# Optimization experiments

Hardware: AMD Instinct MI355X
Metric: run time of the kernel (lower is better)

## Reference

```python
import jax, jax.numpy as jnp
import numpy as np

INPUT_DIM = 1024
OUTPUT_DIM = 1024
DEGREE = 8


def setup_inputs() -> dict:
    key = jax.random.key(0)
    k1, k2 = jax.random.split(key)
    x = jax.random.normal(k1, (8192, INPUT_DIM), dtype=jnp.float32)
    std = 1.0 / (INPUT_DIM * (DEGREE + 1))
    cheby_coeffs = std * jax.random.normal(k2, (INPUT_DIM, OUTPUT_DIM, DEGREE + 1), dtype=jnp.float32)
    return {"x": x, "cheby_coeffs": cheby_coeffs}


def reference(x, cheby_coeffs):
    # x: (B, I); cheby_coeffs: (I, O, D+1)
    degree = cheby_coeffs.shape[-1] - 1
    xt = jnp.tanh(x.reshape(-1, cheby_coeffs.shape[0]))
    # Chebyshev recurrence T_0=1, T_1=x, T_k = 2*x*T_{k-1} - T_{k-2}
    polys = [jnp.ones_like(xt)]
    if degree > 0:
        polys.append(xt)
    for _ in range(2, degree + 1):
        polys.append(2.0 * xt * polys[-1] - polys[-2])
    cheby = jnp.stack(polys, axis=-1)  # (B, I, D+1)
    y = jnp.einsum('bid,iod->bo', cheby, cheby_coeffs)
    return y
```

## Files before the change

kernel.cpp:

```cpp
#include <hip/hip_runtime.h>
#include <hip/hip_bf16.h>

#define AS1 __attribute__((address_space(1)))
#define AS3 __attribute__((address_space(3)))

typedef __attribute__((ext_vector_type(8))) short bf16x8;
typedef __attribute__((ext_vector_type(4))) float f32x4;

#define CSTRIDE 9216
#define KT2 8192
#define NOUT 1024

__device__ __forceinline__ void gll16(const void* g, void* l) {
    __builtin_amdgcn_global_load_lds((const AS1 void*)g, (AS3 void*)l, 16, 0, 0);
}
static __device__ __forceinline__ unsigned short f2bf(float f) {
    union { __hip_bfloat16 h; unsigned short u; } cv;
    cv.h = __float2bfloat16(f);
    return cv.u;
}
static __device__ __forceinline__ float bf2f(unsigned short u) {
    union { float f; unsigned v; } c; c.v = (unsigned)u << 16; return c.f;
}
static __device__ __forceinline__ float fast_tanhf(float v) {
    float e = __expf(2.0f * v);
    return 1.0f - 2.0f / (e + 1.0f);
}

__global__ void __launch_bounds__(256) prep_kernel(const float* __restrict__ cc,
                                                   unsigned short* __restrict__ Wt,
                                                   float* __restrict__ bias) {
    __shared__ unsigned short T[288 * 68];
    const int t  = threadIdx.x;
    const int n0 = (blockIdx.x & 31) * 32;
    const int i0 = (blockIdx.x >> 5) * 64;

    for (int il = 0; il < 64; ++il) {
        const float* src = cc + (size_t)(i0 + il) * CSTRIDE + (size_t)n0 * 9;
        for (int f = t; f < 288; f += 256)
            T[f * 68 + il] = f2bf(src[f]);
    }
    __syncthreads();

#pragma unroll
    for (int it = 0; it < 16; ++it) {
        const int chunk = it * 16 + (t >> 4);
        const int nl = chunk >> 3;
        const int dd = chunk & 7;
        const int n  = n0 + nl;
        const int e0 = (t & 15) * 4;
        const int isrc = e0 ^ ((n & 7) << 3);
        ushort4 v = *(const ushort4*)&T[(nl * 9 + dd + 1) * 68 + isrc];
        *(ushort4*)(Wt + (size_t)n * KT2 + dd * 1024 + i0 + e0) = v;
    }

    if (t < 32) {
        float s = 0.f;
#pragma unroll 8
        for (int il = 0; il < 64; ++il) s += bf2f(T[(t * 9) * 68 + il]);
        atomicAdd(&bias[n0 + t], s);
    }
}

__global__ void __launch_bounds__(256, 2)
cheby_gemm(const float* __restrict__ x, const unsigned short* __restrict__ Wt,
           const float* __restrict__ bias, float* __restrict__ out) {
    __shared__ unsigned short Asub[128 * 64];
    __shared__ unsigned short Bsub[2][128 * 64];

    const int id   = blockIdx.x;
    const int bcol = (id & 7) * 128;
    const int brow = (id >> 3) * 128;
    const int t    = threadIdx.x;
    const int lane = t & 63;
    const int w    = t >> 6;
    const int wr   = (w >> 1) * 64;
    const int wc   = (w & 1) * 64;
    const int l15  = lane & 15;
    const int lhi  = lane >> 4;

    const int gi0 = (t & 15) * 4;
    const int gr  = t >> 4;
    const int bn_loc = t >> 3;
    const int bpos   = (t & 7) * 8;

    unsigned awoff[8];
#pragma unroll
    for (int p = 0; p < 8; ++p) {
        const int r = gr + 16 * p;
        awoff[p] = r * 128 + ((gi0 * 2) ^ ((r & 7) << 4));
    }

    f32x4 acc[4][4] = {};
    float x2[8][4], Tp[8][4], Tpp[8][4];
    float4 xt[8];

#pragma unroll
    for (int p = 0; p < 8; ++p)
        xt[p] = *(const float4*)(x + (size_t)(brow + gr + 16 * p) * 1024 + gi0);
#pragma unroll
    for (int c = 0; c < 4; ++c)
        gll16(Wt + (size_t)(bcol + c * 32 + bn_loc) * KT2 + bpos,
              (char*)Bsub[0] + c * 4096 + w * 1024);

#pragma unroll 1
    for (int ic = 0; ic < 16; ++ic) {
#pragma unroll
        for (int dd = 0; dd < 8; ++dd) {
            const int cur = dd & 1;
            const int nxt = cur ^ 1;
            const int ddn = (dd + 1) & 7;
            const int icn = (dd == 7) ? ((ic + 1) & 15) : ic;
            const int kbn = ddn * 1024 + icn * 64;

            __builtin_amdgcn_s_barrier();

            const bool xpre = (dd == 7) && (ic != 15);
            if (xpre) {
#pragma unroll
                for (int p = 0; p < 8; ++p)
                    xt[p] = *(const float4*)(x + (size_t)(brow + gr + 16 * p) * 1024
                                             + icn * 64 + gi0);
            }

#pragma unroll
            for (int c = 0; c < 4; ++c)
                gll16(Wt + (size_t)(bcol + c * 32 + bn_loc) * KT2 + kbn + bpos,
                      (char*)Bsub[nxt] + c * 4096 + w * 1024);

            if (dd == 0) {
#pragma unroll
                for (int p = 0; p < 8; ++p) {
                    ushort4 pk; unsigned short* pks = (unsigned short*)&pk;
#pragma unroll
                    for (int j = 0; j < 4; ++j) {
                        x2[p][j] = 2.0f * fast_tanhf((&xt[p].x)[j]);
                        const float c = 0.5f * x2[p][j];
                        Tp[p][j] = c; Tpp[p][j] = 1.0f;
                        pks[j] = f2bf(c);
                    }
                    *(ushort4*)((char*)Asub + awoff[p]) = pk;
                }
            } else {
#pragma unroll
                for (int p = 0; p < 8; ++p) {
                    ushort4 pk; unsigned short* pks = (unsigned short*)&pk;
#pragma unroll
                    for (int j = 0; j < 4; ++j) {
                        const float c = __builtin_fmaf(x2[p][j], Tp[p][j], -Tpp[p][j]);
                        Tpp[p][j] = Tp[p][j]; Tp[p][j] = c;
                        pks[j] = f2bf(c);
                    }
                    *(ushort4*)((char*)Asub + awoff[p]) = pk;
                }
            }

            if (xpre) {
                asm volatile("s_waitcnt vmcnt(12) lgkmcnt(0)" ::: "memory");
            } else {
                asm volatile("s_waitcnt vmcnt(4) lgkmcnt(0)" ::: "memory");
            }
            __builtin_amdgcn_s_barrier();

#pragma unroll
            for (int ks = 0; ks < 2; ++ks) {
                bf16x8 af[4], bfr[4];
#pragma unroll
                for (int mf = 0; mf < 4; ++mf) {
                    const int row = wr + mf * 16 + l15;
                    af[mf] = *(const bf16x8*)((const char*)Asub + row * 128 +
                              ((ks * 64 + lhi * 16) ^ ((row & 7) << 4)));
                }
#pragma unroll
                for (int nf = 0; nf < 4; ++nf) {
                    const int n = wc + nf * 16 + l15;
                    bfr[nf] = *(const bf16x8*)((const char*)Bsub[cur] + n * 128 +
                              ((ks * 64 + lhi * 16) ^ ((n & 7) << 4)));
                }
#pragma unroll
                for (int mf = 0; mf < 4; ++mf)
#pragma unroll
                    for (int nf = 0; nf < 4; ++nf)
                        acc[mf][nf] = __builtin_amdgcn_mfma_f32_16x16x32_bf16(
                            af[mf], bfr[nf], acc[mf][nf], 0, 0, 0);
            }
        }
    }

    float bv[4];
#pragma unroll
    for (int nf = 0; nf < 4; ++nf) bv[nf] = bias[bcol + wc + nf * 16 + l15];
#pragma unroll
    for (int mf = 0; mf < 4; ++mf)
#pragma unroll
        for (int nf = 0; nf < 4; ++nf)
#pragma unroll
            for (int ri = 0; ri < 4; ++ri) {
                const int orow = brow + wr + mf * 16 + lhi * 4 + ri;
                const int ocol = bcol + wc + nf * 16 + l15;
                out[(size_t)orow * NOUT + ocol] = acc[mf][nf][ri] + bv[nf];
            }
}

__global__ void __launch_bounds__(256) naive_kernel(const float* __restrict__ x,
                                                    const float* __restrict__ cc,
                                                    float* __restrict__ out) {
    __shared__ float xs[1024];
    const int b = blockIdx.x;
    const int t = threadIdx.x;
#pragma unroll
    for (int j = 0; j < 4; ++j)
        xs[t * 4 + j] = fast_tanhf(x[(size_t)b * 1024 + t * 4 + j]);
    __syncthreads();

    const int o = t * 4;
    float a0 = 0.f, a1 = 0.f, a2 = 0.f, a3 = 0.f;
    for (int i = 0; i < 1024; ++i) {
        const float* cp = cc + (size_t)i * CSTRIDE + (size_t)o * 9;
        const float xv = xs[i];
        float tpp = 1.0f, tp = xv;
        a0 += cp[0];  a1 += cp[9];  a2 += cp[18];  a3 += cp[27];
        a0 += xv * cp[1]; a1 += xv * cp[10]; a2 += xv * cp[19]; a3 += xv * cp[28];
#pragma unroll
        for (int d = 2; d <= 8; ++d) {
            const float cur = 2.0f * xv * tp - tpp;
            tpp = tp; tp = cur;
            a0 += cur * cp[d];      a1 += cur * cp[9 + d];
            a2 += cur * cp[18 + d]; a3 += cur * cp[27 + d];
        }
    }
    float* op = out + (size_t)b * NOUT + o;
    op[0] = a0; op[1] = a1; op[2] = a2; op[3] = a3;
}

extern "C" void kernel_launch(void* const* d_in, const int* in_sizes, int n_in,
                              void* d_out, int out_size, void* d_ws, size_t ws_size,
                              hipStream_t stream) {
    const float* x  = (const float*)d_in[0];
    const float* cc = (const float*)d_in[1];
    float* out = (float*)d_out;

    const size_t wt_bytes = (size_t)KT2 * 1024 * sizeof(unsigned short);
    const size_t need = wt_bytes + 1024 * sizeof(float);
    if (ws_size >= need) {
        unsigned short* Wt = (unsigned short*)d_ws;
        float* bias = (float*)((char*)d_ws + wt_bytes);
        hipMemsetAsync(bias, 0, 1024 * sizeof(float), stream);
        prep_kernel<<<512, 256, 0, stream>>>(cc, Wt, bias);
        cheby_gemm<<<512, 256, 0, stream>>>(x, Wt, bias, out);
    } else {
        naive_kernel<<<8192, 256, 0, stream>>>(x, cc, out);
    }
}
```

Baseline: 274.3 us.

## Shrink GEMM M-tile to 64 and drop B double buffering for occupancy

Halves the row tile of the Chebyshev GEMM to 64, removes the double-buffered B tile and the cross-iteration x prefetch, and launches twice as many blocks with launch bounds raised to 4 waves per SIMD. The aim is to raise occupancy by cutting LDS and register use so that more resident blocks hide latency. In exchange, loads are no longer overlapped within a block, each W tile is fetched twice as often, and every step waits on a full synchronization.

```diff
diff --git a/kernel.cpp b/kernel.cpp
--- a/kernel.cpp
+++ b/kernel.cpp
@@ -62,19 +62,19 @@
     }
 }
 
-__global__ void __launch_bounds__(256, 2)
+__global__ void __launch_bounds__(256, 4)
 cheby_gemm(const float* __restrict__ x, const unsigned short* __restrict__ Wt,
            const float* __restrict__ bias, float* __restrict__ out) {
-    __shared__ unsigned short Asub[128 * 64];
-    __shared__ unsigned short Bsub[2][128 * 64];
+    __shared__ unsigned short Asub[64 * 64];
+    __shared__ unsigned short Bsub[128 * 64];
 
     const int id   = blockIdx.x;
     const int bcol = (id & 7) * 128;
-    const int brow = (id >> 3) * 128;
+    const int brow = (id >> 3) * 64;
     const int t    = threadIdx.x;
     const int lane = t & 63;
     const int w    = t >> 6;
-    const int wr   = (w >> 1) * 64;
+    const int wr   = (w >> 1) * 32;
     const int wc   = (w & 1) * 64;
     const int l15  = lane & 15;
     const int lhi  = lane >> 4;
@@ -84,53 +84,37 @@
     const int bn_loc = t >> 3;
     const int bpos   = (t & 7) * 8;
 
-    unsigned awoff[8];
-#pragma unroll
-    for (int p = 0; p < 8; ++p) {
+    unsigned awoff[4];
+#pragma unroll
+    for (int p = 0; p < 4; ++p) {
         const int r = gr + 16 * p;
         awoff[p] = r * 128 + ((gi0 * 2) ^ ((r & 7) << 4));
     }
 
-    f32x4 acc[4][4] = {};
-    float x2[8][4], Tp[8][4], Tpp[8][4];
-    float4 xt[8];
-
-#pragma unroll
-    for (int p = 0; p < 8; ++p)
-        xt[p] = *(const float4*)(x + (size_t)(brow + gr + 16 * p) * 1024 + gi0);
-#pragma unroll
-    for (int c = 0; c < 4; ++c)
-        gll16(Wt + (size_t)(bcol + c * 32 + bn_loc) * KT2 + bpos,
-              (char*)Bsub[0] + c * 4096 + w * 1024);
+    f32x4 acc[2][4] = {};
+    float x2[4][4], Tp[4][4], Tpp[4][4];
 
 #pragma unroll 1
     for (int ic = 0; ic < 16; ++ic) {
+        float4 xt[4];
+#pragma unroll
+        for (int p = 0; p < 4; ++p)
+            xt[p] = *(const float4*)(x + (size_t)(brow + gr + 16 * p) * 1024
+                                     + ic * 64 + gi0);
+
 #pragma unroll
         for (int dd = 0; dd < 8; ++dd) {
-            const int cur = dd & 1;
-            const int nxt = cur ^ 1;
-            const int ddn = (dd + 1) & 7;
-            const int icn = (dd == 7) ? ((ic + 1) & 15) : ic;
-            const int kbn = ddn * 1024 + icn * 64;
-
-            __builtin_amdgcn_s_barrier();
-
-            const bool xpre = (dd == 7) && (ic != 15);
-            if (xpre) {
-#pragma unroll
-                for (int p = 0; p < 8; ++p)
-                    xt[p] = *(const float4*)(x + (size_t)(brow + gr + 16 * p) * 1024
-                                             + icn * 64 + gi0);
-            }
-
+            __syncthreads();
+
+            const int kb = dd * 1024 + ic * 64;
 #pragma unroll
             for (int c = 0; c < 4; ++c)
-                gll16(Wt + (size_t)(bcol + c * 32 + bn_loc) * KT2 + kbn + bpos,
-                      (char*)Bsub[nxt] + c * 4096 + w * 1024);
+                gll16(Wt + (size_t)(bcol + c * 32 + bn_loc) * KT2 + kb + bpos,
+                      (char*)Bsub + c * 4096 + w * 1024);
 
             if (dd == 0) {
 #pragma unroll
-                for (int p = 0; p < 8; ++p) {
+                for (int p = 0; p < 4; ++p) {
                     ushort4 pk; unsigned short* pks = (unsigned short*)&pk;
 #pragma unroll
                     for (int j = 0; j < 4; ++j) {
@@ -143,7 +127,7 @@
                 }
             } else {
 #pragma unroll
-                for (int p = 0; p < 8; ++p) {
+                for (int p = 0; p < 4; ++p) {
                     ushort4 pk; unsigned short* pks = (unsigned short*)&pk;
 #pragma unroll
                     for (int j = 0; j < 4; ++j) {
@@ -155,18 +139,13 @@
                 }
             }
 
-            if (xpre) {
-                asm volatile("s_waitcnt vmcnt(12) lgkmcnt(0)" ::: "memory");
-            } else {
-                asm volatile("s_waitcnt vmcnt(4) lgkmcnt(0)" ::: "memory");
-            }
-            __builtin_amdgcn_s_barrier();
+            __syncthreads();
 
 #pragma unroll
             for (int ks = 0; ks < 2; ++ks) {
-                bf16x8 af[4], bfr[4];
-#pragma unroll
-                for (int mf = 0; mf < 4; ++mf) {
+                bf16x8 af[2], bfr[4];
+#pragma unroll
+                for (int mf = 0; mf < 2; ++mf) {
                     const int row = wr + mf * 16 + l15;
                     af[mf] = *(const bf16x8*)((const char*)Asub + row * 128 +
                               ((ks * 64 + lhi * 16) ^ ((row & 7) << 4)));
@@ -174,11 +153,11 @@
 #pragma unroll
                 for (int nf = 0; nf < 4; ++nf) {
                     const int n = wc + nf * 16 + l15;
-                    bfr[nf] = *(const bf16x8*)((const char*)Bsub[cur] + n * 128 +
+                    bfr[nf] = *(const bf16x8*)((const char*)Bsub + n * 128 +
                               ((ks * 64 + lhi * 16) ^ ((n & 7) << 4)));
                 }
 #pragma unroll
-                for (int mf = 0; mf < 4; ++mf)
+                for (int mf = 0; mf < 2; ++mf)
 #pragma unroll
                     for (int nf = 0; nf < 4; ++nf)
                         acc[mf][nf] = __builtin_amdgcn_mfma_f32_16x16x32_bf16(
@@ -191,7 +170,7 @@
 #pragma unroll
     for (int nf = 0; nf < 4; ++nf) bv[nf] = bias[bcol + wc + nf * 16 + l15];
 #pragma unroll
-    for (int mf = 0; mf < 4; ++mf)
+    for (int mf = 0; mf < 2; ++mf)
 #pragma unroll
         for (int nf = 0; nf < 4; ++nf)
 #pragma unroll
@@ -247,7 +226,7 @@
         float* bias = (float*)((char*)d_ws + wt_bytes);
         hipMemsetAsync(bias, 0, 1024 * sizeof(float), stream);
         prep_kernel<<<512, 256, 0, stream>>>(cc, Wt, bias);
-        cheby_gemm<<<512, 256, 0, stream>>>(x, Wt, bias, out);
+        cheby_gemm<<<1024, 256, 0, stream>>>(x, Wt, bias, out);
     } else {
         naive_kernel<<<8192, 256, 0, stream>>>(x, cc, out);
     }
```

After: 251.1 us. 1.09x faster.

## Process two Chebyshev degrees per K-step with interleaved weight layout

Applied to the files above, without the earlier changes.

The packed weight layout is reordered so the eight degrees for each 64-input chunk are contiguous, and each GEMM iteration now covers two degrees (K=128) instead of one. This halves the number of barriers and loop iterations and computes two recurrence steps per pass. In exchange it drops the double-buffered B tile and the x prefetch. Weight loads are no longer overlapped with MFMA work, and the loads now sit behind a full __syncthreads, so latency may be exposed.

```diff
diff --git a/kernel.cpp b/kernel.cpp
--- a/kernel.cpp
+++ b/kernel.cpp
@@ -51,7 +51,7 @@
         const int e0 = (t & 15) * 4;
         const int isrc = e0 ^ ((n & 7) << 3);
         ushort4 v = *(const ushort4*)&T[(nl * 9 + dd + 1) * 68 + isrc];
-        *(ushort4*)(Wt + (size_t)n * KT2 + dd * 1024 + i0 + e0) = v;
+        *(ushort4*)(Wt + (size_t)n * KT2 + (i0 >> 6) * 512 + dd * 64 + e0) = v;
     }
 
     if (t < 32) {
@@ -65,8 +65,8 @@
 __global__ void __launch_bounds__(256, 2)
 cheby_gemm(const float* __restrict__ x, const unsigned short* __restrict__ Wt,
            const float* __restrict__ bias, float* __restrict__ out) {
-    __shared__ unsigned short Asub[128 * 64];
-    __shared__ unsigned short Bsub[2][128 * 64];
+    __shared__ unsigned short Asub[128 * 128];
+    __shared__ unsigned short Bsub[128 * 128];
 
     const int id   = blockIdx.x;
     const int bcol = (id & 7) * 128;
@@ -81,101 +81,88 @@
 
     const int gi0 = (t & 15) * 4;
     const int gr  = t >> 4;
-    const int bn_loc = t >> 3;
-    const int bpos   = (t & 7) * 8;
+    const int bn4 = lane >> 4;
+    const int be  = (lane & 15) * 8;
 
     unsigned awoff[8];
 #pragma unroll
     for (int p = 0; p < 8; ++p) {
         const int r = gr + 16 * p;
-        awoff[p] = r * 128 + ((gi0 * 2) ^ ((r & 7) << 4));
+        awoff[p] = r * 256 + ((gi0 * 2) ^ ((r & 7) << 4));
     }
 
     f32x4 acc[4][4] = {};
     float x2[8][4], Tp[8][4], Tpp[8][4];
-    float4 xt[8];
-
-#pragma unroll
-    for (int p = 0; p < 8; ++p)
-        xt[p] = *(const float4*)(x + (size_t)(brow + gr + 16 * p) * 1024 + gi0);
-#pragma unroll
-    for (int c = 0; c < 4; ++c)
-        gll16(Wt + (size_t)(bcol + c * 32 + bn_loc) * KT2 + bpos,
-              (char*)Bsub[0] + c * 4096 + w * 1024);
 
 #pragma unroll 1
     for (int ic = 0; ic < 16; ++ic) {
 #pragma unroll
-        for (int dd = 0; dd < 8; ++dd) {
-            const int cur = dd & 1;
-            const int nxt = cur ^ 1;
-            const int ddn = (dd + 1) & 7;
-            const int icn = (dd == 7) ? ((ic + 1) & 15) : ic;
-            const int kbn = ddn * 1024 + icn * 64;
-
-            __builtin_amdgcn_s_barrier();
-
-            const bool xpre = (dd == 7) && (ic != 15);
-            if (xpre) {
-#pragma unroll
-                for (int p = 0; p < 8; ++p)
-                    xt[p] = *(const float4*)(x + (size_t)(brow + gr + 16 * p) * 1024
-                                             + icn * 64 + gi0);
-            }
-
-#pragma unroll
-            for (int c = 0; c < 4; ++c)
-                gll16(Wt + (size_t)(bcol + c * 32 + bn_loc) * KT2 + kbn + bpos,
-                      (char*)Bsub[nxt] + c * 4096 + w * 1024);
-
-            if (dd == 0) {
+        for (int dp = 0; dp < 4; ++dp) {
+            __syncthreads();
+
+            const int kb = ic * 512 + dp * 128;
+#pragma unroll
+            for (int c = 0; c < 8; ++c) {
+                const int n_base = w * 32 + c * 4;
+                gll16(Wt + (size_t)(bcol + n_base + bn4) * KT2 + kb + be,
+                      (char*)Bsub + n_base * 256);
+            }
+
+            if (dp == 0) {
 #pragma unroll
                 for (int p = 0; p < 8; ++p) {
-                    ushort4 pk; unsigned short* pks = (unsigned short*)&pk;
+                    const float4 v = *(const float4*)(x +
+                        (size_t)(brow + gr + 16 * p) * 1024 + ic * 64 + gi0);
+                    ushort4 pk1, pk2;
+                    unsigned short* s1 = (unsigned short*)&pk1;
+                    unsigned short* s2 = (unsigned short*)&pk2;
 #pragma unroll
                     for (int j = 0; j < 4; ++j) {
-                        x2[p][j] = 2.0f * fast_tanhf((&xt[p].x)[j]);
-                        const float c = 0.5f * x2[p][j];
-                        Tp[p][j] = c; Tpp[p][j] = 1.0f;
-                        pks[j] = f2bf(c);
+                        x2[p][j] = 2.0f * fast_tanhf((&v.x)[j]);
+                        const float t1 = 0.5f * x2[p][j];
+                        const float t2 = __builtin_fmaf(x2[p][j], t1, -1.0f);
+                        Tpp[p][j] = t1; Tp[p][j] = t2;
+                        s1[j] = f2bf(t1); s2[j] = f2bf(t2);
                     }
-                    *(ushort4*)((char*)Asub + awoff[p]) = pk;
+                    *(ushort4*)((char*)Asub + awoff[p]) = pk1;
+                    *(ushort4*)((char*)Asub + awoff[p] + 128) = pk2;
                 }
             } else {
 #pragma unroll
                 for (int p = 0; p < 8; ++p) {
-                    ushort4 pk; unsigned short* pks = (unsigned short*)&pk;
+                    ushort4 pk1, pk2;
+                    unsigned short* s1 = (unsigned short*)&pk1;
+                    unsigned short* s2 = (unsigned short*)&pk2;
 #pragma unroll
                     for (int j = 0; j < 4; ++j) {
-                        const float c = __builtin_fmaf(x2[p][j], Tp[p][j], -Tpp[p][j]);
-                        Tpp[p][j] = Tp[p][j]; Tp[p][j] = c;
-                        pks[j] = f2bf(c);
+                        const float ta = __builtin_fmaf(x2[p][j], Tp[p][j], -Tpp[p][j]);
+                        const float tb = __builtin_fmaf(x2[p][j], ta, -Tp[p][j]);
+                        Tpp[p][j] = ta; Tp[p][j] = tb;
+                        s1[j] = f2bf(ta); s2[j] = f2bf(tb);
                     }
-                    *(ushort4*)((char*)Asub + awoff[p]) = pk;
-                }
-            }
-
-            if (xpre) {
-                asm volatile("s_waitcnt vmcnt(12) lgkmcnt(0)" ::: "memory");
-            } else {
-                asm volatile("s_waitcnt vmcnt(4) lgkmcnt(0)" ::: "memory");
-            }
-            __builtin_amdgcn_s_barrier();
-
-#pragma unroll
-            for (int ks = 0; ks < 2; ++ks) {
+                    *(ushort4*)((char*)Asub + awoff[p]) = pk1;
+                    *(ushort4*)((char*)Asub + awoff[p] + 128) = pk2;
+                }
+            }
+
+            __syncthreads();
+
+#pragma unroll
+            for (int ks = 0; ks < 4; ++ks) {
+                const int koff = (ks >> 1) * 128;
+                const int kin  = (ks & 1) * 64 + lhi * 16;
                 bf16x8 af[4], bfr[4];
 #pragma unroll
                 for (int mf = 0; mf < 4; ++mf) {
                     const int row = wr + mf * 16 + l15;
-                    af[mf] = *(const bf16x8*)((const char*)Asub + row * 128 +
-                              ((ks * 64 + lhi * 16) ^ ((row & 7) << 4)));
+                    af[mf] = *(const bf16x8*)((const char*)Asub + row * 256 +
+                              koff + (kin ^ ((row & 7) << 4)));
                 }
 #pragma unroll
                 for (int nf = 0; nf < 4; ++nf) {
                     const int n = wc + nf * 16 + l15;
-                    bfr[nf] = *(const bf16x8*)((const char*)Bsub[cur] + n * 128 +
-                              ((ks * 64 + lhi * 16) ^ ((n & 7) << 4)));
+                    bfr[nf] = *(const bf16x8*)((const char*)Bsub + n * 256 +
+                              koff + (kin ^ ((n & 7) << 4)));
                 }
 #pragma unroll
                 for (int mf = 0; mf < 4; ++mf)
```

Result: slower. 284.2 us (+3.6%).
